# Performance work log

Hardware: AMD Instinct MI355X
Metric: run time of the kernel (lower is better)

## Reference

```python
import jax, jax.numpy as jnp
import numpy as np

D_MODEL = 1024
N_HEADS = 16
HEAD_DIM = D_MODEL // N_HEADS


def setup_inputs() -> dict:
    key = jax.random.key(0)
    ks = jax.random.split(key, 9)
    B, S = 4, 2048
    x = jax.random.normal(ks[0], (B, S, D_MODEL), dtype=jnp.float32)
    init = 1.0 / np.sqrt(D_MODEL)
    def lin(kw, kb):
        W = jax.random.uniform(kw, (D_MODEL, D_MODEL), jnp.float32, -init, init)
        b = jax.random.uniform(kb, (D_MODEL,), jnp.float32, -init, init)
        return W, b
    Wq, bq = lin(ks[1], ks[2])
    Wk, bk = lin(ks[3], ks[4])
    Wv, bv = lin(ks[5], ks[6])
    Wo, bo = lin(ks[7], ks[8])
    return {"x": x, "Wq": Wq, "bq": bq, "Wk": Wk, "bk": bk,
            "Wv": Wv, "bv": bv, "Wo": Wo, "bo": bo}


def reference(x, Wq, bq, Wk, bk, Wv, bv, Wo, bo):
    B, S, _ = x.shape
    scale = jnp.sqrt(jnp.float32(HEAD_DIM))
    def split_heads(t):  # [B,S,D] -> [B,H,S,hd]
        return t.reshape(B, S, N_HEADS, HEAD_DIM).transpose(0, 2, 1, 3)
    q = split_heads(x @ Wq.T + bq)
    k = split_heads(x @ Wk.T + bk)
    v = split_heads(x @ Wv.T + bv)
    attn = jnp.einsum('bhqd,bhkd->bhqk', q, k) / scale
    attn = jax.nn.softmax(attn, axis=-1)
    out = jnp.einsum('bhqk,bhkd->bhqd', attn, v)  # [B,H,S,hd]
    out = out.transpose(0, 2, 1, 3).reshape(B, S, D_MODEL)
    return out @ Wo.T + bo
```

## Files before the change

kernel.cpp:

```cpp
#include <hip/hip_runtime.h>
#include <hip/hip_bf16.h>
#include <stdint.h>

typedef __attribute__((ext_vector_type(8))) short bf16x8;
typedef __attribute__((ext_vector_type(4))) float f32x4;
typedef __attribute__((ext_vector_type(16))) float f32x16;
typedef __attribute__((ext_vector_type(2))) unsigned int u32x2;
typedef unsigned short u16;

#define DEVI static __device__ __forceinline__

DEVI u16 f2bf(float f) {
  union { float f; uint32_t u; } x; x.f = f;
  uint32_t r = (x.u + 0x7FFFu + ((x.u >> 16) & 1u)) >> 16;
  return (u16)r;
}

DEVI void gload_lds16(const void* g, void* lds) {
  __builtin_amdgcn_global_load_lds(
      (const __attribute__((address_space(1))) void*)(void*)g,
      (__attribute__((address_space(3))) void*)lds, 16, 0, 0);
}

DEVI unsigned ldsaddr(const void* p) { return (unsigned)(uintptr_t)p; }

__global__ void cvt_all_kernel(const float* __restrict__ x,
                               const float* __restrict__ Wq, const float* __restrict__ Wk,
                               const float* __restrict__ Wv, const float* __restrict__ Wo,
                               const float* __restrict__ bq, const float* __restrict__ bk,
                               const float* __restrict__ bv,
                               u16* __restrict__ xb, u16* __restrict__ Wqkvb,
                               u16* __restrict__ Wob, float* __restrict__ bqkv) {
  const int X4 = 2097152;
  const int W4 = 262144;
  const int total = X4 + 4 * W4 + 768;
  int i = blockIdx.x * blockDim.x + threadIdx.x;
  const int stride = gridDim.x * blockDim.x;
  for (; i < total; i += stride) {
    if (i < X4) {
      float4 v = ((const float4*)x)[i];
      ((ushort4*)xb)[i] = make_ushort4(f2bf(v.x), f2bf(v.y), f2bf(v.z), f2bf(v.w));
    } else if (i < X4 + 4 * W4) {
      int j = i - X4;
      int which = j >> 18;
      int o = j & (W4 - 1);
      const float* src = which == 0 ? Wq : which == 1 ? Wk : which == 2 ? Wv : Wo;
      u16* dst = (which == 3) ? Wob : (Wqkvb + (size_t)which * 1048576);
      float4 v = ((const float4*)src)[o];
      ((ushort4*)dst)[o] = make_ushort4(f2bf(v.x), f2bf(v.y), f2bf(v.z), f2bf(v.w));
    } else {
      int j = i - X4 - 4 * W4;
      int which = j >> 8;
      int o = j & 255;
      const float* src = which == 0 ? bq : which == 1 ? bk : bv;
      ((float4*)bqkv)[which * 256 + o] = ((const float4*)src)[o];
    }
  }
}

template<int OUT_BF16>
__global__ __launch_bounds__(256, 2)
void gemm_bt_kernel(const u16* __restrict__ A, const u16* __restrict__ B,
                    const float* __restrict__ bias, void* __restrict__ C,
                    int M, int N, int K, int scale_cols, float scale_val) {
  __shared__ u16 As[128 * 32];
  __shared__ u16 Bs[128 * 32];
  const int tid = threadIdx.x;
  const int l = tid & 63;
  const int w = tid >> 6;
  const int bm = blockIdx.y, bn = blockIdx.x;
  const int wm = w >> 1, wn = w & 1;

  f32x4 acc[4][4] = {};

  const int srow = w * 32 + (l >> 2);
  const int scol = (l & 3) * 8;
  const u16* gA0 = A + (size_t)(bm * 128 + srow) * K + scol;
  const u16* gA1 = gA0 + (size_t)16 * K;
  const u16* gB0 = B + (size_t)(bn * 128 + srow) * K + scol;
  const u16* gB1 = gB0 + (size_t)16 * K;
  u16* lA0 = As + w * 1024;
  u16* lA1 = As + w * 1024 + 512;
  u16* lB0 = Bs + w * 1024;
  u16* lB1 = Bs + w * 1024 + 512;

  const int ar = wm * 64 + (l & 15);
  const int br = wn * 64 + (l & 15);
  const int kb = (l >> 4) * 8;

  for (int k0 = 0; k0 < K; k0 += 32) {
    __syncthreads();
    gload_lds16(gA0 + k0, lA0);
    gload_lds16(gA1 + k0, lA1);
    gload_lds16(gB0 + k0, lB0);
    gload_lds16(gB1 + k0, lB1);
    __syncthreads();
    bf16x8 af[4], bfr[4];
#pragma unroll
    for (int mf = 0; mf < 4; ++mf)
      af[mf] = *(const bf16x8*)&As[(ar + mf * 16) * 32 + kb];
#pragma unroll
    for (int nf = 0; nf < 4; ++nf)
      bfr[nf] = *(const bf16x8*)&Bs[(br + nf * 16) * 32 + kb];
#pragma unroll
    for (int mf = 0; mf < 4; ++mf)
#pragma unroll
      for (int nf = 0; nf < 4; ++nf)
        acc[mf][nf] = __builtin_amdgcn_mfma_f32_16x16x32_bf16(af[mf], bfr[nf], acc[mf][nf], 0, 0, 0);
  }

  const int rbase = bm * 128 + wm * 64 + (l >> 4) * 4;
  const int cbase = bn * 128 + wn * 64 + (l & 15);
#pragma unroll
  for (int nf = 0; nf < 4; ++nf) {
    int col = cbase + nf * 16;
    float bsv = bias[col];
    float sc = (col < scale_cols) ? scale_val : 1.0f;
#pragma unroll
    for (int mf = 0; mf < 4; ++mf) {
#pragma unroll
      for (int j = 0; j < 4; ++j) {
        int row = rbase + mf * 16 + j;
        float v = (acc[mf][nf][j] + bsv) * sc;
        if (OUT_BF16) ((u16*)C)[(size_t)row * N + col] = f2bf(v);
        else          ((float*)C)[(size_t)row * N + col] = v;
      }
    }
  }
}

DEVI void softmax_pa(f32x16& sA, f32x16& sB, bf16x8* pa, float& lsum, int hi) {
  float rs = 0.f;
#pragma unroll
  for (int r = 0; r < 16; ++r) { sA[r] = __builtin_amdgcn_exp2f(sA[r]); rs += sA[r]; }
#pragma unroll
  for (int r = 0; r < 16; ++r) { sB[r] = __builtin_amdgcn_exp2f(sB[r]); rs += sB[r]; }
  lsum += rs + __shfl_xor(rs, 32, 64);
#pragma unroll
  for (int i = 0; i < 4; ++i) {
    float p0 = (8 * i + 0 < 16) ? sA[(8 * i + 0) & 15] : sB[(8 * i + 0) & 15];
    float p1 = (8 * i + 1 < 16) ? sA[(8 * i + 1) & 15] : sB[(8 * i + 1) & 15];
    float p2 = (8 * i + 2 < 16) ? sA[(8 * i + 2) & 15] : sB[(8 * i + 2) & 15];
    float p3 = (8 * i + 3 < 16) ? sA[(8 * i + 3) & 15] : sB[(8 * i + 3) & 15];
    float p4 = (8 * i + 4 < 16) ? sA[(8 * i + 4) & 15] : sB[(8 * i + 4) & 15];
    float p5 = (8 * i + 5 < 16) ? sA[(8 * i + 5) & 15] : sB[(8 * i + 5) & 15];
    float p6 = (8 * i + 6 < 16) ? sA[(8 * i + 6) & 15] : sB[(8 * i + 6) & 15];
    float p7 = (8 * i + 7 < 16) ? sA[(8 * i + 7) & 15] : sB[(8 * i + 7) & 15];
    unsigned a0, a1, b0, b1;
    asm("v_cvt_pk_bf16_f32 %0, %1, %2" : "=v"(a0) : "v"(p0), "v"(p1));
    asm("v_cvt_pk_bf16_f32 %0, %1, %2" : "=v"(a1) : "v"(p2), "v"(p3));
    asm("v_cvt_pk_bf16_f32 %0, %1, %2" : "=v"(b0) : "v"(p4), "v"(p5));
    asm("v_cvt_pk_bf16_f32 %0, %1, %2" : "=v"(b1) : "v"(p6), "v"(p7));
    unsigned t0 = hi ? a0 : b0;
    unsigned t1 = hi ? a1 : b1;
    unsigned x0 = (unsigned)__shfl_xor((int)t0, 32, 64);
    unsigned x1 = (unsigned)__shfl_xor((int)t1, 32, 64);
    union { unsigned u[4]; bf16x8 v; } U;
    U.u[0] = hi ? x0 : a0;
    U.u[1] = hi ? x1 : a1;
    U.u[2] = hi ? b0 : x0;
    U.u[3] = hi ? b1 : x1;
    pa[i] = U.v;
  }
}

__global__ __launch_bounds__(256, 2)
void attn_kernel(const u16* __restrict__ QKV, u16* __restrict__ O) {
  __shared__ u16 Ks[3][4096];
  __shared__ u16 Vs[3][4096];

  const int tid = threadIdx.x;
  const int l = tid & 63, w = tid >> 6;
  const int hi = l >> 5, c = l & 31;
  const int bh = blockIdx.y, b = bh >> 4, h = bh & 15;
  const int qb = blockIdx.x * 256 + w * 64;
  const size_t rowbase = (size_t)b * 2048;

  bf16x8 qf0[4], qf1[4];
  {
    const u16* Qp0 = QKV + (rowbase + qb + c) * 3072 + h * 64 + hi * 8;
    const u16* Qp1 = QKV + (rowbase + qb + 32 + c) * 3072 + h * 64 + hi * 8;
#pragma unroll
    for (int kk = 0; kk < 4; ++kk) {
      qf0[kk] = *(const bf16x8*)(Qp0 + kk * 16);
      qf1[kk] = *(const bf16x8*)(Qp1 + kk * 16);
    }
  }

  const int kd0 = (w * 2 + 0) * 64 + l;
  const int kd1 = (w * 2 + 1) * 64 + l;
  const int rK0 = kd0 >> 3, dbK0 = (kd0 & 7) ^ (rK0 & 7);
  const int rK1 = kd1 >> 3, dbK1 = (kd1 & 7) ^ (rK1 & 7);
  const u16* srcK0 = QKV + (rowbase + rK0) * 3072 + 1024 + h * 64 + dbK0 * 8;
  const u16* srcK1 = QKV + (rowbase + rK1) * 3072 + 1024 + h * 64 + dbK1 * 8;
  const int kV0 = (kd0 >> 5) * 4 + ((kd0 >> 1) & 3), dV0 = ((kd0 >> 3) & 3) * 16 + (kd0 & 1) * 8;
  const int kV1 = (kd1 >> 5) * 4 + ((kd1 >> 1) & 3), dV1 = ((kd1 >> 3) & 3) * 16 + (kd1 & 1) * 8;
  const u16* srcV0 = QKV + (rowbase + kV0) * 3072 + 2048 + h * 64 + dV0;
  const u16* srcV1 = QKV + (rowbase + kV1) * 3072 + 2048 + h * 64 + dV1;

#define STAGE(buf, tile) { \
    const size_t koff = (size_t)(tile) * 64 * 3072; \
    gload_lds16(srcK0 + koff, &Ks[buf][(w * 2 + 0) * 512]); \
    gload_lds16(srcK1 + koff, &Ks[buf][(w * 2 + 1) * 512]); \
    gload_lds16(srcV0 + koff, &Vs[buf][(w * 2 + 0) * 512]); \
    gload_lds16(srcV1 + koff, &Vs[buf][(w * 2 + 1) * 512]); \
  }

  int koffs[4];
#pragma unroll
  for (int kk = 0; kk < 4; ++kk) koffs[kk] = (((kk * 2 + hi) ^ (c & 7)) * 8);
  const int kbase = c * 64;

  const unsigned vbase = ldsaddr(&Vs[0][0]) + (unsigned)(hi * 1024 + (c >> 4) * 128 + (c & 15) * 8);

  f32x16 o00 = {0,0,0,0,0,0,0,0,0,0,0,0,0,0,0,0};
  f32x16 o01 = {0,0,0,0,0,0,0,0,0,0,0,0,0,0,0,0};
  f32x16 o10 = {0,0,0,0,0,0,0,0,0,0,0,0,0,0,0,0};
  f32x16 o11 = {0,0,0,0,0,0,0,0,0,0,0,0,0,0,0,0};
  float lsum0 = 0.f, lsum1 = 0.f;

  STAGE(0, 0);
  STAGE(1, 1);

  int cur = 0;
  for (int t = 0; t < 32; ++t) {
    if (t < 31) { asm volatile("s_waitcnt vmcnt(4)" ::: "memory"); }
    else        { asm volatile("s_waitcnt vmcnt(0)" ::: "memory"); }
    __builtin_amdgcn_s_barrier();
    asm volatile("" ::: "memory");

    if (t < 30) {
      int bs = cur + 2; if (bs >= 3) bs -= 3;
      STAGE(bs, t + 2);
    }

    const u16* kp = &Ks[cur][0];
    bf16x8 kf[2][4];
#pragma unroll
    for (int kb = 0; kb < 2; ++kb)
#pragma unroll
      for (int kk = 0; kk < 4; ++kk)
        kf[kb][kk] = *(const bf16x8*)&kp[kbase + kb * 2048 + koffs[kk]];

    f32x16 sA0 = {0,0,0,0,0,0,0,0,0,0,0,0,0,0,0,0};
    f32x16 sB0 = {0,0,0,0,0,0,0,0,0,0,0,0,0,0,0,0};
    f32x16 sA1 = {0,0,0,0,0,0,0,0,0,0,0,0,0,0,0,0};
    f32x16 sB1 = {0,0,0,0,0,0,0,0,0,0,0,0,0,0,0,0};
#pragma unroll
    for (int kk = 0; kk < 4; ++kk) {
      sA0 = __builtin_amdgcn_mfma_f32_32x32x16_bf16(kf[0][kk], qf0[kk], sA0, 0, 0, 0);
      sB0 = __builtin_amdgcn_mfma_f32_32x32x16_bf16(kf[1][kk], qf0[kk], sB0, 0, 0, 0);
      sA1 = __builtin_amdgcn_mfma_f32_32x32x16_bf16(kf[0][kk], qf1[kk], sA1, 0, 0, 0);
      sB1 = __builtin_amdgcn_mfma_f32_32x32x16_bf16(kf[1][kk], qf1[kk], sB1, 0, 0, 0);
    }

    const unsigned va = vbase + (unsigned)(cur * 8192);
    u32x2 tt[4][4];
#pragma unroll
    for (int ks = 0; ks < 4; ++ks) {
      unsigned va_ks = va + (unsigned)(ks * 2048);
      asm volatile("ds_read_b64_tr_b16 %0, %1 offset:0"   : "=v"(tt[ks][0]) : "v"(va_ks));
      asm volatile("ds_read_b64_tr_b16 %0, %1 offset:512" : "=v"(tt[ks][1]) : "v"(va_ks));
      asm volatile("ds_read_b64_tr_b16 %0, %1 offset:256" : "=v"(tt[ks][2]) : "v"(va_ks));
      asm volatile("ds_read_b64_tr_b16 %0, %1 offset:768" : "=v"(tt[ks][3]) : "v"(va_ks));
    }

    bf16x8 pa0[4];
    softmax_pa(sA0, sB0, pa0, lsum0, hi);

    asm volatile("s_waitcnt lgkmcnt(0)" ::: "memory");
    __builtin_amdgcn_sched_barrier(0);

#pragma unroll
    for (int ks = 0; ks < 4; ++ks) {
      union { u32x2 d2[2]; bf16x8 v; } V0, V1;
      V0.d2[0] = tt[ks][0]; V0.d2[1] = tt[ks][1];
      V1.d2[0] = tt[ks][2]; V1.d2[1] = tt[ks][3];
      o00 = __builtin_amdgcn_mfma_f32_32x32x16_bf16(pa0[ks], V0.v, o00, 0, 0, 0);
      o01 = __builtin_amdgcn_mfma_f32_32x32x16_bf16(pa0[ks], V1.v, o01, 0, 0, 0);
    }

    bf16x8 pa1[4];
    softmax_pa(sA1, sB1, pa1, lsum1, hi);

#pragma unroll
    for (int ks = 0; ks < 4; ++ks) {
      union { u32x2 d2[2]; bf16x8 v; } V0, V1;
      V0.d2[0] = tt[ks][0]; V0.d2[1] = tt[ks][1];
      V1.d2[0] = tt[ks][2]; V1.d2[1] = tt[ks][3];
      o10 = __builtin_amdgcn_mfma_f32_32x32x16_bf16(pa1[ks], V0.v, o10, 0, 0, 0);
      o11 = __builtin_amdgcn_mfma_f32_32x32x16_bf16(pa1[ks], V1.v, o11, 0, 0, 0);
    }

    asm volatile("" ::: "memory");
    cur = (cur == 2) ? 0 : cur + 1;
  }

  u16* Op0 = O + (rowbase + qb) * 1024 + h * 64 + c;
  u16* Op1 = O + (rowbase + qb + 32) * 1024 + h * 64 + c;
#pragma unroll
  for (int r = 0; r < 16; ++r) {
    int q = (r & 3) + 8 * (r >> 2) + 4 * hi;
    float inv0 = 1.0f / __shfl(lsum0, q, 64);
    float inv1 = 1.0f / __shfl(lsum1, q, 64);
    Op0[(size_t)q * 1024]      = f2bf(o00[r] * inv0);
    Op0[(size_t)q * 1024 + 32] = f2bf(o01[r] * inv0);
    Op1[(size_t)q * 1024]      = f2bf(o10[r] * inv1);
    Op1[(size_t)q * 1024 + 32] = f2bf(o11[r] * inv1);
  }
#undef STAGE
}

extern "C" void kernel_launch(void* const* d_in, const int* in_sizes, int n_in,
                              void* d_out, int out_size, void* d_ws, size_t ws_size,
                              hipStream_t stream) {
  const float* x  = (const float*)d_in[0];
  const float* Wq = (const float*)d_in[1];
  const float* bq = (const float*)d_in[2];
  const float* Wk = (const float*)d_in[3];
  const float* bk = (const float*)d_in[4];
  const float* Wv = (const float*)d_in[5];
  const float* bv = (const float*)d_in[6];
  const float* Wo = (const float*)d_in[7];
  const float* bo = (const float*)d_in[8];
  float* out = (float*)d_out;

  char* ws = (char*)d_ws;
  u16*   xb    = (u16*)(ws);
  u16*   Wqkvb = (u16*)(ws + 16777216);
  u16*   Wob   = (u16*)(ws + 23068672);
  float* bqkv  = (float*)(ws + 25165824);
  u16*   QKV   = (u16*)(ws + 25178112);
  u16*   Oa    = (u16*)(ws + 75509760);

  cvt_all_kernel<<<2048, 256, 0, stream>>>(x, Wq, Wk, Wv, Wo, bq, bk, bv,
                                           xb, Wqkvb, Wob, bqkv);

  gemm_bt_kernel<1><<<dim3(24, 64), 256, 0, stream>>>(xb, Wqkvb, bqkv, QKV,
                                                      8192, 3072, 1024, 1024,
                                                      0.125f * 1.4426950408889634f);
  attn_kernel<<<dim3(8, 64), 256, 0, stream>>>(QKV, Oa);
  gemm_bt_kernel<0><<<dim3(8, 64), 256, 0, stream>>>(Oa, Wob, bo, out,
                                                     8192, 1024, 1024, 0, 1.0f);
}
```

Baseline: 196.0 us.

## Software-pipeline QK^T one tile ahead with four-stage K/V LDS ring

Restructures the attention main loop so the QK^T MFMAs for tile t+1 are issued while softmax and PV for tile t run, with a prologue computing the first scores and an epilogue draining the last tile. The K/V LDS ring grows from three to four buffers with prefetch three tiles ahead, and V transpose reads are issued before the barrier. This aims to hide softmax VALU latency and LDS/global latency behind matrix-core work. It costs more LDS (64KB per block) and more live score registers, which may hurt occupancy at two blocks per CU.

Measured after the change: 201.0 us. 1.03x slower.

```diff
diff --git a/kernel.cpp b/kernel.cpp
--- a/kernel.cpp
+++ b/kernel.cpp
@@ -166,8 +166,8 @@
 
 __global__ __launch_bounds__(256, 2)
 void attn_kernel(const u16* __restrict__ QKV, u16* __restrict__ O) {
-  __shared__ u16 Ks[3][4096];
-  __shared__ u16 Vs[3][4096];
+  __shared__ u16 Ks[4][4096];
+  __shared__ u16 Vs[4][4096];
 
   const int tid = threadIdx.x;
   const int l = tid & 63, w = tid >> 6;
@@ -213,87 +213,121 @@
 
   const unsigned vbase = ldsaddr(&Vs[0][0]) + (unsigned)(hi * 1024 + (c >> 4) * 128 + (c & 15) * 8);
 
+#define VTR_ISSUE(va, tt) { \
+    _Pragma("unroll") \
+    for (int ks = 0; ks < 4; ++ks) { \
+      unsigned va_ks = (va) + (unsigned)(ks * 2048); \
+      asm volatile("ds_read_b64_tr_b16 %0, %1 offset:0"   : "=v"(tt[ks][0]) : "v"(va_ks)); \
+      asm volatile("ds_read_b64_tr_b16 %0, %1 offset:512" : "=v"(tt[ks][1]) : "v"(va_ks)); \
+      asm volatile("ds_read_b64_tr_b16 %0, %1 offset:256" : "=v"(tt[ks][2]) : "v"(va_ks)); \
+      asm volatile("ds_read_b64_tr_b16 %0, %1 offset:768" : "=v"(tt[ks][3]) : "v"(va_ks)); \
+    } \
+  }
+
+#define PV_GROUP(pa, oL, oH) { \
+    _Pragma("unroll") \
+    for (int ks = 0; ks < 4; ++ks) { \
+      union { u32x2 d2[2]; bf16x8 v; } V0, V1; \
+      V0.d2[0] = tt[ks][0]; V0.d2[1] = tt[ks][1]; \
+      V1.d2[0] = tt[ks][2]; V1.d2[1] = tt[ks][3]; \
+      oL = __builtin_amdgcn_mfma_f32_32x32x16_bf16(pa[ks], V0.v, oL, 0, 0, 0); \
+      oH = __builtin_amdgcn_mfma_f32_32x32x16_bf16(pa[ks], V1.v, oH, 0, 0, 0); \
+    } \
+  }
+
   f32x16 o00 = {0,0,0,0,0,0,0,0,0,0,0,0,0,0,0,0};
   f32x16 o01 = {0,0,0,0,0,0,0,0,0,0,0,0,0,0,0,0};
   f32x16 o10 = {0,0,0,0,0,0,0,0,0,0,0,0,0,0,0,0};
   f32x16 o11 = {0,0,0,0,0,0,0,0,0,0,0,0,0,0,0,0};
   float lsum0 = 0.f, lsum1 = 0.f;
 
+  f32x16 sA0, sB0, sA1, sB1;
+
   STAGE(0, 0);
   STAGE(1, 1);
-
-  int cur = 0;
-  for (int t = 0; t < 32; ++t) {
-    if (t < 31) { asm volatile("s_waitcnt vmcnt(4)" ::: "memory"); }
+  STAGE(2, 2);
+  asm volatile("s_waitcnt vmcnt(8)" ::: "memory");
+  __builtin_amdgcn_s_barrier();
+  asm volatile("" ::: "memory");
+  {
+    const u16* kp = &Ks[0][0];
+    f32x16 z = {0,0,0,0,0,0,0,0,0,0,0,0,0,0,0,0};
+    sA0 = z; sB0 = z; sA1 = z; sB1 = z;
+    bf16x8 kfA[4];
+#pragma unroll
+    for (int kk = 0; kk < 4; ++kk) kfA[kk] = *(const bf16x8*)&kp[kbase + koffs[kk]];
+#pragma unroll
+    for (int kk = 0; kk < 4; ++kk) {
+      sA0 = __builtin_amdgcn_mfma_f32_32x32x16_bf16(kfA[kk], qf0[kk], sA0, 0, 0, 0);
+      sA1 = __builtin_amdgcn_mfma_f32_32x32x16_bf16(kfA[kk], qf1[kk], sA1, 0, 0, 0);
+    }
+#pragma unroll
+    for (int kk = 0; kk < 4; ++kk) kfA[kk] = *(const bf16x8*)&kp[kbase + 2048 + koffs[kk]];
+#pragma unroll
+    for (int kk = 0; kk < 4; ++kk) {
+      sB0 = __builtin_amdgcn_mfma_f32_32x32x16_bf16(kfA[kk], qf0[kk], sB0, 0, 0, 0);
+      sB1 = __builtin_amdgcn_mfma_f32_32x32x16_bf16(kfA[kk], qf1[kk], sB1, 0, 0, 0);
+    }
+  }
+
+  for (int t = 0; t < 31; ++t) {
+    u32x2 tt[4][4];
+    const unsigned va = vbase + (unsigned)((t & 3) * 8192);
+    VTR_ISSUE(va, tt);
+
+    if (t < 30) { asm volatile("s_waitcnt vmcnt(4)" ::: "memory"); }
     else        { asm volatile("s_waitcnt vmcnt(0)" ::: "memory"); }
     __builtin_amdgcn_s_barrier();
     asm volatile("" ::: "memory");
-
-    if (t < 30) {
-      int bs = cur + 2; if (bs >= 3) bs -= 3;
-      STAGE(bs, t + 2);
-    }
-
-    const u16* kp = &Ks[cur][0];
-    bf16x8 kf[2][4];
-#pragma unroll
-    for (int kb = 0; kb < 2; ++kb)
-#pragma unroll
-      for (int kk = 0; kk < 4; ++kk)
-        kf[kb][kk] = *(const bf16x8*)&kp[kbase + kb * 2048 + koffs[kk]];
-
-    f32x16 sA0 = {0,0,0,0,0,0,0,0,0,0,0,0,0,0,0,0};
-    f32x16 sB0 = {0,0,0,0,0,0,0,0,0,0,0,0,0,0,0,0};
-    f32x16 sA1 = {0,0,0,0,0,0,0,0,0,0,0,0,0,0,0,0};
-    f32x16 sB1 = {0,0,0,0,0,0,0,0,0,0,0,0,0,0,0,0};
-#pragma unroll
-    for (int kk = 0; kk < 4; ++kk) {
-      sA0 = __builtin_amdgcn_mfma_f32_32x32x16_bf16(kf[0][kk], qf0[kk], sA0, 0, 0, 0);
-      sB0 = __builtin_amdgcn_mfma_f32_32x32x16_bf16(kf[1][kk], qf0[kk], sB0, 0, 0, 0);
-      sA1 = __builtin_amdgcn_mfma_f32_32x32x16_bf16(kf[0][kk], qf1[kk], sA1, 0, 0, 0);
-      sB1 = __builtin_amdgcn_mfma_f32_32x32x16_bf16(kf[1][kk], qf1[kk], sB1, 0, 0, 0);
-    }
-
-    const unsigned va = vbase + (unsigned)(cur * 8192);
-    u32x2 tt[4][4];
-#pragma unroll
-    for (int ks = 0; ks < 4; ++ks) {
-      unsigned va_ks = va + (unsigned)(ks * 2048);
-      asm volatile("ds_read_b64_tr_b16 %0, %1 offset:0"   : "=v"(tt[ks][0]) : "v"(va_ks));
-      asm volatile("ds_read_b64_tr_b16 %0, %1 offset:512" : "=v"(tt[ks][1]) : "v"(va_ks));
-      asm volatile("ds_read_b64_tr_b16 %0, %1 offset:256" : "=v"(tt[ks][2]) : "v"(va_ks));
-      asm volatile("ds_read_b64_tr_b16 %0, %1 offset:768" : "=v"(tt[ks][3]) : "v"(va_ks));
-    }
-
-    bf16x8 pa0[4];
+    if (t <= 28) STAGE((t + 3) & 3, t + 3);
+
+    bf16x8 pa0[4], pa1[4];
     softmax_pa(sA0, sB0, pa0, lsum0, hi);
+    softmax_pa(sA1, sB1, pa1, lsum1, hi);
+
+    const u16* kp = &Ks[(t + 1) & 3][0];
+    f32x16 nA0 = {0,0,0,0,0,0,0,0,0,0,0,0,0,0,0,0};
+    f32x16 nB0 = {0,0,0,0,0,0,0,0,0,0,0,0,0,0,0,0};
+    f32x16 nA1 = {0,0,0,0,0,0,0,0,0,0,0,0,0,0,0,0};
+    f32x16 nB1 = {0,0,0,0,0,0,0,0,0,0,0,0,0,0,0,0};
+    {
+      bf16x8 kf[4];
+#pragma unroll
+      for (int kk = 0; kk < 4; ++kk) kf[kk] = *(const bf16x8*)&kp[kbase + koffs[kk]];
+#pragma unroll
+      for (int kk = 0; kk < 4; ++kk) {
+        nA0 = __builtin_amdgcn_mfma_f32_32x32x16_bf16(kf[kk], qf0[kk], nA0, 0, 0, 0);
+        nA1 = __builtin_amdgcn_mfma_f32_32x32x16_bf16(kf[kk], qf1[kk], nA1, 0, 0, 0);
+      }
+#pragma unroll
+      for (int kk = 0; kk < 4; ++kk) kf[kk] = *(const bf16x8*)&kp[kbase + 2048 + koffs[kk]];
+#pragma unroll
+      for (int kk = 0; kk < 4; ++kk) {
+        nB0 = __builtin_amdgcn_mfma_f32_32x32x16_bf16(kf[kk], qf0[kk], nB0, 0, 0, 0);
+        nB1 = __builtin_amdgcn_mfma_f32_32x32x16_bf16(kf[kk], qf1[kk], nB1, 0, 0, 0);
+      }
+    }
 
     asm volatile("s_waitcnt lgkmcnt(0)" ::: "memory");
     __builtin_amdgcn_sched_barrier(0);
-
-#pragma unroll
-    for (int ks = 0; ks < 4; ++ks) {
-      union { u32x2 d2[2]; bf16x8 v; } V0, V1;
-      V0.d2[0] = tt[ks][0]; V0.d2[1] = tt[ks][1];
-      V1.d2[0] = tt[ks][2]; V1.d2[1] = tt[ks][3];
-      o00 = __builtin_amdgcn_mfma_f32_32x32x16_bf16(pa0[ks], V0.v, o00, 0, 0, 0);
-      o01 = __builtin_amdgcn_mfma_f32_32x32x16_bf16(pa0[ks], V1.v, o01, 0, 0, 0);
-    }
-
-    bf16x8 pa1[4];
+    PV_GROUP(pa0, o00, o01);
+    PV_GROUP(pa1, o10, o11);
+
+    sA0 = nA0; sB0 = nB0; sA1 = nA1; sB1 = nB1;
+    asm volatile("" ::: "memory");
+  }
+
+  {
+    u32x2 tt[4][4];
+    const unsigned va = vbase + (unsigned)(3 * 8192);
+    VTR_ISSUE(va, tt);
+    bf16x8 pa0[4], pa1[4];
+    softmax_pa(sA0, sB0, pa0, lsum0, hi);
     softmax_pa(sA1, sB1, pa1, lsum1, hi);
-
-#pragma unroll
-    for (int ks = 0; ks < 4; ++ks) {
-      union { u32x2 d2[2]; bf16x8 v; } V0, V1;
-      V0.d2[0] = tt[ks][0]; V0.d2[1] = tt[ks][1];
-      V1.d2[0] = tt[ks][2]; V1.d2[1] = tt[ks][3];
-      o10 = __builtin_amdgcn_mfma_f32_32x32x16_bf16(pa1[ks], V0.v, o10, 0, 0, 0);
-      o11 = __builtin_amdgcn_mfma_f32_32x32x16_bf16(pa1[ks], V1.v, o11, 0, 0, 0);
-    }
-
-    asm volatile("" ::: "memory");
-    cur = (cur == 2) ? 0 : cur + 1;
+    asm volatile("s_waitcnt lgkmcnt(0)" ::: "memory");
+    __builtin_amdgcn_sched_barrier(0);
+    PV_GROUP(pa0, o00, o01);
+    PV_GROUP(pa1, o10, o11);
   }
 
   u16* Op0 = O + (rowbase + qb) * 1024 + h * 64 + c;
@@ -309,6 +343,8 @@
     Op1[(size_t)q * 1024 + 32] = f2bf(o11[r] * inv1);
   }
 #undef STAGE
+#undef VTR_ISSUE
+#undef PV_GROUP
 }
 
 extern "C" void kernel_launch(void* const* d_in, const int* in_sizes, int n_in,
```

## Rewrite projection GEMM with 8-wave 128x256 tiles, double-buffered swizzled LDS

Applied to the files above, without the earlier changes.

Replaces the 4-wave 128x128 GEMM with an 8-wave kernel computing 128x256 tiles using K-step 64. Global-to-LDS loads go into a double buffer so the next K tile is prefetched while MFMAs run on the current one. The LDS layout is XOR-swizzled to avoid bank conflicts. Interleaved barriers and setprio are added to stagger waves. This targets the QKV and output projections' load latency and LDS traffic. The cost is more LDS per block (96KB) and fewer blocks in the grid, which may lower occupancy.

Result: slower. 213.9 us (+9.1%).

```diff
diff --git a/kernel.cpp b/kernel.cpp
--- a/kernel.cpp
+++ b/kernel.cpp
@@ -59,58 +59,98 @@
 }
 
 template<int OUT_BF16>
-__global__ __launch_bounds__(256, 2)
-void gemm_bt_kernel(const u16* __restrict__ A, const u16* __restrict__ B,
-                    const float* __restrict__ bias, void* __restrict__ C,
-                    int M, int N, int K, int scale_cols, float scale_val) {
-  __shared__ u16 As[128 * 32];
-  __shared__ u16 Bs[128 * 32];
+__global__ __launch_bounds__(512, 2)
+void gemm_bt8_kernel(const u16* __restrict__ A, const u16* __restrict__ B,
+                     const float* __restrict__ bias, void* __restrict__ C,
+                     int M, int N, int K, int scale_cols, float scale_val) {
+  __shared__ u16 As[2][8192];
+  __shared__ u16 Bs[2][16384];
   const int tid = threadIdx.x;
   const int l = tid & 63;
   const int w = tid >> 6;
-  const int bm = blockIdx.y, bn = blockIdx.x;
-  const int wm = w >> 1, wn = w & 1;
+  const int wm = w >> 2, wn = w & 3;
+  const int bn = blockIdx.x, bm = blockIdx.y;
+
+  const int trow = tid >> 3;
+  const int lc = (tid & 7) ^ (trow & 7);
+  const u16* gA0 = A + (size_t)(bm * 128 + trow) * K + lc * 8;
+  const u16* gA1 = gA0 + (size_t)64 * K;
+  const u16* gB0 = B + (size_t)(bn * 256 + trow) * K + lc * 8;
+  const u16* gB1 = gB0 + (size_t)64 * K;
+  const u16* gB2 = gB0 + (size_t)128 * K;
+  const u16* gB3 = gB0 + (size_t)192 * K;
+
+#define GSTAGE(d, kt) { \
+    const size_t ko = (size_t)(kt) * 64; \
+    gload_lds16(gA0 + ko, &As[d][tid * 8]); \
+    gload_lds16(gA1 + ko, &As[d][4096 + tid * 8]); \
+    gload_lds16(gB0 + ko, &Bs[d][tid * 8]); \
+    gload_lds16(gB1 + ko, &Bs[d][4096 + tid * 8]); \
+    gload_lds16(gB2 + ko, &Bs[d][8192 + tid * 8]); \
+    gload_lds16(gB3 + ko, &Bs[d][12288 + tid * 8]); \
+  }
+
+  const int arow = (wm * 64 + (l & 15)) * 64;
+  const int brow = (wn * 64 + (l & 15)) * 64;
+  int coff[2];
+#pragma unroll
+  for (int kk = 0; kk < 2; ++kk) coff[kk] = (((kk * 4 + (l >> 4)) ^ (l & 7)) * 8);
 
   f32x4 acc[4][4] = {};
-
-  const int srow = w * 32 + (l >> 2);
-  const int scol = (l & 3) * 8;
-  const u16* gA0 = A + (size_t)(bm * 128 + srow) * K + scol;
-  const u16* gA1 = gA0 + (size_t)16 * K;
-  const u16* gB0 = B + (size_t)(bn * 128 + srow) * K + scol;
-  const u16* gB1 = gB0 + (size_t)16 * K;
-  u16* lA0 = As + w * 1024;
-  u16* lA1 = As + w * 1024 + 512;
-  u16* lB0 = Bs + w * 1024;
-  u16* lB1 = Bs + w * 1024 + 512;
-
-  const int ar = wm * 64 + (l & 15);
-  const int br = wn * 64 + (l & 15);
-  const int kb = (l >> 4) * 8;
-
-  for (int k0 = 0; k0 < K; k0 += 32) {
-    __syncthreads();
-    gload_lds16(gA0 + k0, lA0);
-    gload_lds16(gA1 + k0, lA1);
-    gload_lds16(gB0 + k0, lB0);
-    gload_lds16(gB1 + k0, lB1);
-    __syncthreads();
-    bf16x8 af[4], bfr[4];
-#pragma unroll
-    for (int mf = 0; mf < 4; ++mf)
-      af[mf] = *(const bf16x8*)&As[(ar + mf * 16) * 32 + kb];
+  const int NT = K >> 6;
+
+  GSTAGE(0, 0);
+
+  for (int kt = 0; kt < NT; ++kt) {
+    const int cur = kt & 1;
+    asm volatile("s_waitcnt vmcnt(0)" ::: "memory");
+    __builtin_amdgcn_s_barrier();
+    asm volatile("" ::: "memory");
+    if (kt < NT - 1) GSTAGE(cur ^ 1, kt + 1);
+
+    const u16* ap = &As[cur][0];
+    const u16* bp = &Bs[cur][0];
+
+    bf16x8 bf[4][2], af[2];
 #pragma unroll
     for (int nf = 0; nf < 4; ++nf)
-      bfr[nf] = *(const bf16x8*)&Bs[(br + nf * 16) * 32 + kb];
-#pragma unroll
-    for (int mf = 0; mf < 4; ++mf)
+#pragma unroll
+      for (int kk = 0; kk < 2; ++kk)
+        bf[nf][kk] = *(const bf16x8*)&bp[brow + nf * 1024 + coff[kk]];
+#pragma unroll
+    for (int kk = 0; kk < 2; ++kk) af[kk] = *(const bf16x8*)&ap[arow + coff[kk]];
+    asm volatile("s_waitcnt lgkmcnt(0)" ::: "memory");
+    __builtin_amdgcn_sched_barrier(0);
+    __builtin_amdgcn_s_setprio(1);
+#pragma unroll
+    for (int kk = 0; kk < 2; ++kk)
 #pragma unroll
       for (int nf = 0; nf < 4; ++nf)
-        acc[mf][nf] = __builtin_amdgcn_mfma_f32_16x16x32_bf16(af[mf], bfr[nf], acc[mf][nf], 0, 0, 0);
+        acc[0][nf] = __builtin_amdgcn_mfma_f32_16x16x32_bf16(af[kk], bf[nf][kk], acc[0][nf], 0, 0, 0);
+    __builtin_amdgcn_s_setprio(0);
+    __builtin_amdgcn_s_barrier();
+
+#pragma unroll
+    for (int mf = 1; mf < 4; ++mf) {
+#pragma unroll
+      for (int kk = 0; kk < 2; ++kk)
+        af[kk] = *(const bf16x8*)&ap[arow + mf * 1024 + coff[kk]];
+      asm volatile("s_waitcnt lgkmcnt(0)" ::: "memory");
+      __builtin_amdgcn_sched_barrier(0);
+      __builtin_amdgcn_s_setprio(1);
+#pragma unroll
+      for (int kk = 0; kk < 2; ++kk)
+#pragma unroll
+        for (int nf = 0; nf < 4; ++nf)
+          acc[mf][nf] = __builtin_amdgcn_mfma_f32_16x16x32_bf16(af[kk], bf[nf][kk], acc[mf][nf], 0, 0, 0);
+      __builtin_amdgcn_s_setprio(0);
+      if (mf < 3) __builtin_amdgcn_s_barrier();
+    }
+    asm volatile("" ::: "memory");
   }
 
   const int rbase = bm * 128 + wm * 64 + (l >> 4) * 4;
-  const int cbase = bn * 128 + wn * 64 + (l & 15);
+  const int cbase = bn * 256 + wn * 64 + (l & 15);
 #pragma unroll
   for (int nf = 0; nf < 4; ++nf) {
     int col = cbase + nf * 16;
@@ -127,6 +167,7 @@
       }
     }
   }
+#undef GSTAGE
 }
 
 DEVI void softmax_pa(f32x16& sA, f32x16& sB, bf16x8* pa, float& lsum, int hi) {
@@ -336,10 +377,10 @@
   cvt_all_kernel<<<2048, 256, 0, stream>>>(x, Wq, Wk, Wv, Wo, bq, bk, bv,
                                            xb, Wqkvb, Wob, bqkv);
 
-  gemm_bt_kernel<1><<<dim3(24, 64), 256, 0, stream>>>(xb, Wqkvb, bqkv, QKV,
-                                                      8192, 3072, 1024, 1024,
-                                                      0.125f * 1.4426950408889634f);
+  gemm_bt8_kernel<1><<<dim3(12, 64), 512, 0, stream>>>(xb, Wqkvb, bqkv, QKV,
+                                                       8192, 3072, 1024, 1024,
+                                                       0.125f * 1.4426950408889634f);
   attn_kernel<<<dim3(8, 64), 256, 0, stream>>>(QKV, Oa);
-  gemm_bt_kernel<0><<<dim3(8, 64), 256, 0, stream>>>(Oa, Wob, bo, out,
-                                                     8192, 1024, 1024, 0, 1.0f);
-}
+  gemm_bt8_kernel<0><<<dim3(4, 64), 512, 0, stream>>>(Oa, Wob, bo, out,
+                                                      8192, 1024, 1024, 0, 1.0f);
+}
```
